# Performance work log

Measured on AMD Instinct MI355X. Metric: run time of the kernel, lower is better.

Reference implementation:

```python
import jax, jax.numpy as jnp
import numpy as np

HIDDEN = 1024
N_HEAD = 16
HEAD_DIM = HIDDEN // N_HEAD

def setup_inputs() -> dict:
    key = jax.random.key(0)
    ks = jax.random.split(key, 5)
    B, T = 2, 2048
    s_in = 1.0 / np.sqrt(HIDDEN)
    return {
        "x": jax.random.normal(ks[0], (B, T, HIDDEN), dtype=jnp.float32),
        "w_attn": jax.random.normal(ks[1], (HIDDEN, 3 * HIDDEN), dtype=jnp.float32) * s_in,
        "b_attn": jnp.zeros((3 * HIDDEN,), dtype=jnp.float32),
        "w_proj": jax.random.normal(ks[2], (HIDDEN, HIDDEN), dtype=jnp.float32) * s_in,
        "b_proj": jnp.zeros((HIDDEN,), dtype=jnp.float32),
    }

def reference(x, w_attn, b_attn, w_proj, b_proj):
    B, T, C = x.shape
    qkv = x @ w_attn + b_attn  # (B, T, 3C)
    q, k, v = jnp.split(qkv, 3, axis=-1)
    # (B, H, T, D)
    q = q.reshape(B, T, N_HEAD, HEAD_DIM).transpose(0, 2, 1, 3)
    k = k.reshape(B, T, N_HEAD, HEAD_DIM).transpose(0, 2, 1, 3)
    v = v.reshape(B, T, N_HEAD, HEAD_DIM).transpose(0, 2, 1, 3)
    scale = 1.0 / np.sqrt(HEAD_DIM).astype(np.float32)
    attn = jnp.einsum('bhqd,bhkd->bhqk', q, k) * scale
    causal = jnp.tril(jnp.ones((T, T), dtype=bool))
    attn = jnp.where(causal[None, None], attn, -jnp.inf)
    attn = jax.nn.softmax(attn, axis=-1)
    out = jnp.einsum('bhqk,bhkd->bhqd', attn, v)
    out = out.transpose(0, 2, 1, 3).reshape(B, T, C)
    return out @ w_proj + b_proj
```

## Files before the change

### kernel.cpp

```cpp
#include <hip/hip_runtime.h>
#include <stdint.h>

#define T_SEQ 2048
#define NB 2
#define NH 16
#define HD 64
#define HID 1024
#define MTOK (NB * T_SEQ)

typedef float f32x4 __attribute__((ext_vector_type(4)));
typedef float f32x16 __attribute__((ext_vector_type(16)));
typedef short bf16x8 __attribute__((ext_vector_type(8)));
typedef unsigned short u16;
typedef unsigned int u32;

#define QSCALE 0.1803368801f

__device__ __forceinline__ u16 f2bf(float f) {
  union { float f; uint32_t u; } v; v.f = f;
  return (u16)((v.u + 0x7fffu + ((v.u >> 16) & 1u)) >> 16);
}

__device__ __forceinline__ void gl_lds16(const void* g, void* l) {
  __builtin_amdgcn_global_load_lds(
      (const __attribute__((address_space(1))) unsigned int*)g,
      (__attribute__((address_space(3))) unsigned int*)l, 16, 0, 0);
}

__global__ __launch_bounds__(256)
void prep_k(const float* __restrict__ x, u16* __restrict__ xb,
            const float* __restrict__ wa, u16* __restrict__ waT,
            const float* __restrict__ wp, u16* __restrict__ wpT) {
  __shared__ float tile[32][33];
  const int bid = blockIdx.x, tid = threadIdx.x;
  if (bid < 1024) {
    int i = bid * 1024 + tid;
#pragma unroll
    for (int it = 0; it < 4; ++it, i += 256) {
      float4 f = ((const float4*)x)[i];
      ushort4 o;
      o.x = f2bf(f.x); o.y = f2bf(f.y); o.z = f2bf(f.z); o.w = f2bf(f.w);
      ((ushort4*)xb)[i] = o;
    }
    return;
  }
  const float* in;
  u16* out;
  int R, C, c0, r0;
  if (bid < 4096) {
    const int j = bid - 1024;
    in = wa; out = waT; R = HID; C = 3 * HID;
    c0 = (j % 96) * 32; r0 = (j / 96) * 32;
  } else {
    const int j = bid - 4096;
    in = wp; out = wpT; R = HID; C = HID;
    c0 = (j % 32) * 32; r0 = (j / 32) * 32;
  }
  const int tx = tid & 31, ty = tid >> 5;
#pragma unroll
  for (int i = 0; i < 32; i += 8)
    tile[ty + i][tx] = in[(size_t)(r0 + ty + i) * C + c0 + tx];
  __syncthreads();
#pragma unroll
  for (int i = 0; i < 32; i += 8)
    out[(size_t)(c0 + ty + i) * R + r0 + tx] = f2bf(tile[tx][ty + i]);
}

__global__ __launch_bounds__(512, 4)
void gemm_k(const u16* __restrict__ A, const u16* __restrict__ Bt,
            const float* __restrict__ bias,
            u16* __restrict__ q, u16* __restrict__ kk, u16* __restrict__ v) {
  __shared__ __align__(16) char lds[65536];
  const int tid = threadIdx.x, wid = tid >> 6, lane = tid & 63;
  const int bid = blockIdx.y * 24 + blockIdx.x;
  const int xcd = bid & 7, idx = bid >> 3;
  const int m0 = ((xcd >> 1) * 8 + idx / 12) * 128;
  const int n0 = ((xcd & 1) * 12 + idx % 12) * 128;
  const int wm = (wid >> 2) * 64, wn = (wid & 3) * 32;

  f32x4 acc[4][2];
  const f32x4 z = {0.f, 0.f, 0.f, 0.f};
#pragma unroll
  for (int mi = 0; mi < 4; ++mi)
#pragma unroll
    for (int ni = 0; ni < 2; ++ni) acc[mi][ni] = z;

  const int srow = tid >> 3;
  const int scsrc = ((((tid & 7) << 4) ^ ((srow & 7) << 4)) >> 1);
  const int rA = lane & 15;
  const int kg16 = (lane >> 4) << 4;

#define GSTAGE(tt_)                                                                     \
  do {                                                                                  \
    const int k0_ = (tt_) << 6;                                                         \
    char* base_ = lds + (((tt_) & 1) << 15);                                            \
    gl_lds16(A + (size_t)(m0 + srow) * HID + k0_ + scsrc, base_ + wid * 1024);          \
    gl_lds16(A + (size_t)(m0 + 64 + srow) * HID + k0_ + scsrc, base_ + 8192 + wid * 1024); \
    gl_lds16(Bt + (size_t)(n0 + srow) * HID + k0_ + scsrc, base_ + 16384 + wid * 1024); \
    gl_lds16(Bt + (size_t)(n0 + 64 + srow) * HID + k0_ + scsrc, base_ + 24576 + wid * 1024); \
  } while (0)

  GSTAGE(0);
  GSTAGE(1);

  for (int tt = 0; tt < 16; ++tt) {
    if (tt < 15) asm volatile("s_waitcnt vmcnt(4)" ::: "memory");
    else         asm volatile("s_waitcnt vmcnt(0)" ::: "memory");
    __builtin_amdgcn_s_barrier();
    __builtin_amdgcn_sched_barrier(0);

    const char* ab = lds + ((tt & 1) << 15);
    const char* bb = ab + 16384;
#pragma unroll
    for (int ks = 0; ks < 2; ++ks) {
      bf16x8 a[4], b[2];
#pragma unroll
      for (int mi = 0; mi < 4; ++mi) {
        const int row = wm + mi * 16 + rA;
        a[mi] = *(const bf16x8*)(ab + row * 128 + ((ks * 64 + kg16) ^ ((row & 7) << 4)));
      }
#pragma unroll
      for (int ni = 0; ni < 2; ++ni) {
        const int row = wn + ni * 16 + rA;
        b[ni] = *(const bf16x8*)(bb + row * 128 + ((ks * 64 + kg16) ^ ((row & 7) << 4)));
      }
#pragma unroll
      for (int mi = 0; mi < 4; ++mi)
#pragma unroll
        for (int ni = 0; ni < 2; ++ni)
          acc[mi][ni] = __builtin_amdgcn_mfma_f32_16x16x32_bf16(a[mi], b[ni], acc[mi][ni], 0, 0, 0);
    }

    __builtin_amdgcn_s_barrier();
    __builtin_amdgcn_sched_barrier(0);
    if (tt + 2 < 16) GSTAGE(tt + 2);
  }
#undef GSTAGE

  const int coll = lane & 15, rowl = (lane >> 4) << 2;
  const int reg = n0 >> 10;
  const int bb2 = m0 >> 11;
  const int tloc = (m0 & 2047) + wm;
  if (reg == 2) {
#pragma unroll
    for (int mi = 0; mi < 4; ++mi) {
#pragma unroll
      for (int ni = 0; ni < 2; ++ni) {
        const int n = n0 + wn + ni * 16 + coll;
        const float bv = bias[n];
        const int c = n & 1023, h = c >> 6, d = c & 63;
        ushort4 pk;
        pk.x = f2bf(acc[mi][ni][0] + bv);
        pk.y = f2bf(acc[mi][ni][1] + bv);
        pk.z = f2bf(acc[mi][ni][2] + bv);
        pk.w = f2bf(acc[mi][ni][3] + bv);
        const int t0 = tloc + mi * 16 + rowl;
        *(ushort4*)(v + ((size_t)(bb2 * NH + h) * HD + d) * T_SEQ + t0) = pk;
      }
    }
  } else {
    u16* dst = (reg == 0) ? q : kk;
    const float sc = (reg == 0) ? QSCALE : 1.0f;
#pragma unroll
    for (int mi = 0; mi < 4; ++mi) {
#pragma unroll
      for (int ni = 0; ni < 2; ++ni) {
        const int n = n0 + wn + ni * 16 + coll;
        const float bv = bias[n];
        const int c = n & 1023, h = c >> 6, d = c & 63;
#pragma unroll
        for (int r = 0; r < 4; ++r) {
          const int t = tloc + mi * 16 + rowl + r;
          dst[((size_t)(bb2 * NH + h) * T_SEQ + t) * HD + d] = f2bf((acc[mi][ni][r] + bv) * sc);
        }
      }
    }
  }
}

__global__ __launch_bounds__(512, 6)
void gemm2_k(const u16* __restrict__ A, const u16* __restrict__ Bt,
             const float* __restrict__ bias, float* __restrict__ outf) {
  __shared__ __align__(16) char lds[49152];
  const int tid = threadIdx.x, wid = tid >> 6, lane = tid & 63;
  const int m0 = blockIdx.y * 64, n0 = blockIdx.x * 128;
  const int wm = (wid >> 2) * 32, wn = (wid & 3) * 32;

  f32x4 acc[2][2];
  const f32x4 z = {0.f, 0.f, 0.f, 0.f};
#pragma unroll
  for (int mi = 0; mi < 2; ++mi)
#pragma unroll
    for (int ni = 0; ni < 2; ++ni) acc[mi][ni] = z;

  const int srow = tid >> 3;
  const int scsrc = ((((tid & 7) << 4) ^ ((srow & 7) << 4)) >> 1);
  const int rA = lane & 15;
  const int kg16 = (lane >> 4) << 4;

#define G2STAGE(tt_)                                                                    \
  do {                                                                                  \
    const int k0_ = (tt_) << 6;                                                         \
    char* base_ = lds + (((tt_) & 1) ? 24576 : 0);                                      \
    gl_lds16(A + (size_t)(m0 + srow) * HID + k0_ + scsrc, base_ + wid * 1024);          \
    gl_lds16(Bt + (size_t)(n0 + srow) * HID + k0_ + scsrc, base_ + 8192 + wid * 1024);  \
    gl_lds16(Bt + (size_t)(n0 + 64 + srow) * HID + k0_ + scsrc, base_ + 16384 + wid * 1024); \
  } while (0)

  G2STAGE(0);
  G2STAGE(1);

  for (int tt = 0; tt < 16; ++tt) {
    if (tt < 15) asm volatile("s_waitcnt vmcnt(3)" ::: "memory");
    else         asm volatile("s_waitcnt vmcnt(0)" ::: "memory");
    __builtin_amdgcn_s_barrier();
    __builtin_amdgcn_sched_barrier(0);

    const char* ab = lds + ((tt & 1) ? 24576 : 0);
    const char* bb = ab + 8192;
#pragma unroll
    for (int ks = 0; ks < 2; ++ks) {
      bf16x8 a[2], b[2];
#pragma unroll
      for (int mi = 0; mi < 2; ++mi) {
        const int row = wm + mi * 16 + rA;
        a[mi] = *(const bf16x8*)(ab + row * 128 + ((ks * 64 + kg16) ^ ((row & 7) << 4)));
      }
#pragma unroll
      for (int ni = 0; ni < 2; ++ni) {
        const int row = wn + ni * 16 + rA;
        b[ni] = *(const bf16x8*)(bb + row * 128 + ((ks * 64 + kg16) ^ ((row & 7) << 4)));
      }
#pragma unroll
      for (int mi = 0; mi < 2; ++mi)
#pragma unroll
        for (int ni = 0; ni < 2; ++ni)
          acc[mi][ni] = __builtin_amdgcn_mfma_f32_16x16x32_bf16(a[mi], b[ni], acc[mi][ni], 0, 0, 0);
    }

    __builtin_amdgcn_s_barrier();
    __builtin_amdgcn_sched_barrier(0);
    if (tt + 2 < 16) G2STAGE(tt + 2);
  }
#undef G2STAGE

  const int coll = lane & 15, rowl = (lane >> 4) << 2;
#pragma unroll
  for (int mi = 0; mi < 2; ++mi) {
#pragma unroll
    for (int ni = 0; ni < 2; ++ni) {
      const int n = n0 + wn + ni * 16 + coll;
      const float bv = bias[n];
#pragma unroll
      for (int r = 0; r < 4; ++r) {
        const int m = m0 + wm + mi * 16 + rowl + r;
        outf[(size_t)m * HID + n] = acc[mi][ni][r] + bv;
      }
    }
  }
}

__global__ __launch_bounds__(512, 4)
void attn_k(const u16* __restrict__ Q, const u16* __restrict__ K,
            const u16* __restrict__ Vt, u16* __restrict__ AO) {
  __shared__ __align__(16) char lds[65536];
  const int tid = threadIdx.x;
  const int lane = tid & 63;
  const int wid = tid >> 6;
  const int qsub = wid & 3, par = wid >> 2;
  const int bid = blockIdx.x;
  const int halfg = bid >> 8, r8 = bid & 255;
  const int bh = (r8 & 7) * 4 + ((r8 >> 3) & 3);
  const int lvl = r8 >> 5;
  const int qb = halfg ? lvl : (15 - lvl);
  const int q0 = qb * 128;
  const int ql = lane & 31, h = lane >> 5;
  const bool hi = (h != 0);

  const u16* Qg = Q + (size_t)bh * T_SEQ * HD;
  const u16* Kg = K + (size_t)bh * T_SEQ * HD;
  const u16* Vg = Vt + (size_t)bh * T_SEQ * HD;

  const int q0w = q0 + qsub * 32;
  const int dq = 2 * qb + (qsub >> 1);

  bf16x8 qf[4];
#pragma unroll
  for (int s = 0; s < 4; ++s)
    qf[s] = *(const bf16x8*)(Qg + (size_t)(q0w + ql) * HD + s * 16 + h * 8);

  f32x16 ot0, ot1;
#pragma unroll
  for (int i = 0; i < 16; ++i) { ot0[i] = 0.f; ot1[i] = 0.f; }
  float m = -3.0e38f, l = 0.f;

  const int srow = tid >> 3;
  const int scb = (tid & 7) << 4;
  const int sc0 = (scb ^ ((srow & 7) << 4)) >> 1;

  const int nsup = qb + 1;

#define STAGE(tt_)                                                            \
  do {                                                                        \
    const int kv0_ = (tt_) << 6;                                              \
    gl_lds16(Kg + (size_t)(kv0_ + srow) * HD + sc0,                           \
             lds + (((tt_) & 3) << 13) + wid * 1024);                         \
    gl_lds16(Vg + (size_t)srow * T_SEQ + kv0_ + sc0,                          \
             lds + 32768 + (((tt_) & 3) << 13) + wid * 1024);                 \
  } while (0)

  STAGE(0);
  STAGE(1);

  for (int ss = 0; ss < nsup; ++ss) {
    if (ss + 1 < nsup) {
      STAGE(2 * ss + 2);
      STAGE(2 * ss + 3);
      asm volatile("s_waitcnt vmcnt(4)" ::: "memory");
    } else {
      asm volatile("s_waitcnt vmcnt(0)" ::: "memory");
    }
    __builtin_amdgcn_s_barrier();
    __builtin_amdgcn_sched_barrier(0);

    const int tt = 2 * ss + par;
    if (tt <= dq) {
      const int kv0 = tt << 6;
      const char* kb = lds + ((tt & 3) << 13);
      const char* vb = lds + 32768 + ((tt & 3) << 13);
      f32x16 s0, s1;
#pragma unroll
      for (int i = 0; i < 16; ++i) { s0[i] = 0.f; s1[i] = 0.f; }
      __builtin_amdgcn_s_setprio(1);
#pragma unroll
      for (int s = 0; s < 4; ++s) {
        const int cb = 32 * s + 16 * h;
        const int r0 = ql, r1 = 32 + ql;
        bf16x8 kf0 = *(const bf16x8*)(kb + r0 * 128 + (cb ^ ((r0 & 7) << 4)));
        bf16x8 kf1 = *(const bf16x8*)(kb + r1 * 128 + (cb ^ ((r1 & 7) << 4)));
        s0 = __builtin_amdgcn_mfma_f32_32x32x16_bf16(kf0, qf[s], s0, 0, 0, 0);
        s1 = __builtin_amdgcn_mfma_f32_32x32x16_bf16(kf1, qf[s], s1, 0, 0, 0);
      }
      __builtin_amdgcn_s_setprio(0);
      if (tt == dq) {
        const int qg = q0w + ql;
#pragma unroll
        for (int r = 0; r < 16; ++r) {
          const int kvl = (r & 3) + 8 * (r >> 2) + 4 * h;
          if (kv0 + kvl > qg) s0[r] = -3.0e38f;
          if (kv0 + 32 + kvl > qg) s1[r] = -3.0e38f;
        }
      }
      float mx[16];
#pragma unroll
      for (int i = 0; i < 16; ++i) mx[i] = fmaxf(s0[i], s1[i]);
#pragma unroll
      for (int d = 8; d; d >>= 1)
#pragma unroll
        for (int i = 0; i < d; ++i) mx[i] = fmaxf(mx[i], mx[i + d]);
      const float tm = fmaxf(mx[0], __shfl_xor(mx[0], 32, 64));
      if (!__all(tm <= m + 4.0f)) {
        const float mnew = fmaxf(m, tm);
        const float fold = __builtin_amdgcn_exp2f(m - mnew);
        m = mnew;
        l *= fold;
#pragma unroll
        for (int i = 0; i < 16; ++i) { ot0[i] *= fold; ot1[i] *= fold; }
      }
#pragma unroll
      for (int i = 0; i < 16; ++i) {
        s0[i] = __builtin_amdgcn_exp2f(s0[i] - m);
        s1[i] = __builtin_amdgcn_exp2f(s1[i] - m);
      }
      float sm[16];
#pragma unroll
      for (int i = 0; i < 16; ++i) sm[i] = s0[i] + s1[i];
#pragma unroll
      for (int d = 8; d; d >>= 1)
#pragma unroll
        for (int i = 0; i < d; ++i) sm[i] += sm[i + d];
      l += sm[0] + __shfl_xor(sm[0], 32, 64);

      u32 w0[8], w1[8];
#pragma unroll
      for (int mm = 0; mm < 8; ++mm) {
        asm("v_cvt_pk_bf16_f32 %0, %1, %2" : "=v"(w0[mm]) : "v"(s0[2 * mm]), "v"(s0[2 * mm + 1]));
        asm("v_cvt_pk_bf16_f32 %0, %1, %2" : "=v"(w1[mm]) : "v"(s1[2 * mm]), "v"(s1[2 * mm + 1]));
      }
      __builtin_amdgcn_s_setprio(1);
#pragma unroll
      for (int sb = 0; sb < 2; ++sb) {
#pragma unroll
        for (int t = 0; t < 2; ++t) {
          u32 a0 = sb ? w1[4 * t]     : w0[4 * t];
          u32 a1 = sb ? w1[4 * t + 1] : w0[4 * t + 1];
          u32 a2 = sb ? w1[4 * t + 2] : w0[4 * t + 2];
          u32 a3 = sb ? w1[4 * t + 3] : w0[4 * t + 3];
          u32 snd0 = hi ? a0 : a2;
          u32 snd1 = hi ? a1 : a3;
          u32 own0 = hi ? a2 : a0;
          u32 own1 = hi ? a3 : a1;
          u32 p0 = __shfl_xor(snd0, 32, 64);
          u32 p1 = __shfl_xor(snd1, 32, 64);
          union { u32 u[4]; bf16x8 v; } fr;
          fr.u[0] = hi ? p0 : own0;
          fr.u[1] = hi ? p1 : own1;
          fr.u[2] = hi ? own0 : p0;
          fr.u[3] = hi ? own1 : p1;
          const int s = sb * 2 + t;
          const int cb = 32 * s + 16 * h;
          const int r0 = ql, r1 = 32 + ql;
          bf16x8 vf0 = *(const bf16x8*)(vb + r0 * 128 + (cb ^ ((r0 & 7) << 4)));
          bf16x8 vf1 = *(const bf16x8*)(vb + r1 * 128 + (cb ^ ((r1 & 7) << 4)));
          ot0 = __builtin_amdgcn_mfma_f32_32x32x16_bf16(vf0, fr.v, ot0, 0, 0, 0);
          ot1 = __builtin_amdgcn_mfma_f32_32x32x16_bf16(vf1, fr.v, ot1, 0, 0, 0);
        }
      }
      __builtin_amdgcn_s_setprio(0);
    }
    __builtin_amdgcn_s_barrier();
    __builtin_amdgcn_sched_barrier(0);
  }
#undef STAGE

  float* R = (float*)(lds + qsub * 8448);
  if (par == 1) {
#pragma unroll
    for (int r = 0; r < 16; ++r) {
      const int dl = (r & 3) + 8 * (r >> 2) + 4 * h;
      R[ql * 66 + dl] = ot0[r];
      R[ql * 66 + 32 + dl] = ot1[r];
    }
    if (!hi) { R[ql * 66 + 64] = m; R[ql * 66 + 65] = l; }
  }
  __builtin_amdgcn_s_barrier();
  if (par == 1) return;

  const float m2 = R[ql * 66 + 64];
  const float l2 = R[ql * 66 + 65];
  const float M = fmaxf(m, m2);
  const float c1 = __builtin_amdgcn_exp2f(m - M);
  const float c2 = __builtin_amdgcn_exp2f(m2 - M);
  const float L = c1 * l + c2 * l2;
  const float inv = 1.0f / L;
  float of0[16], of1[16];
#pragma unroll
  for (int r = 0; r < 16; ++r) {
    const int dl = (r & 3) + 8 * (r >> 2) + 4 * h;
    of0[r] = (c1 * ot0[r] + c2 * R[ql * 66 + dl]) * inv;
    of1[r] = (c1 * ot1[r] + c2 * R[ql * 66 + 32 + dl]) * inv;
  }
  asm volatile("s_waitcnt lgkmcnt(0)" ::: "memory");
  __builtin_amdgcn_sched_barrier(0);

  float* E = (float*)(lds + qsub * 8448);
#pragma unroll
  for (int r = 0; r < 16; ++r) {
    const int dl = (r & 3) + 8 * (r >> 2) + 4 * h;
    E[dl * 33 + ql] = of0[r];
    E[(dl + 32) * 33 + ql] = of1[r];
  }
  asm volatile("s_waitcnt lgkmcnt(0)" ::: "memory");
  __builtin_amdgcn_sched_barrier(0);
  const int bb = bh >> 4, hh = bh & 15;
  const int r2 = lane >> 3;
  const int c8 = (lane & 7) * 8;
#pragma unroll
  for (int g = 0; g < 4; ++g) {
    const int qrow = g * 8 + r2;
    union { u16 a[8]; bf16x8 v; } ov;
#pragma unroll
    for (int j = 0; j < 8; ++j) ov.a[j] = f2bf(E[(c8 + j) * 33 + qrow]);
    *(bf16x8*)(AO + (size_t)(bb * T_SEQ + q0 + qsub * 32 + qrow) * HID + hh * HD + c8) = ov.v;
  }
}

extern "C" void kernel_launch(void* const* d_in, const int* in_sizes, int n_in,
                              void* d_out, int out_size, void* d_ws, size_t ws_size,
                              hipStream_t stream) {
  const float* x      = (const float*)d_in[0];
  const float* w_attn = (const float*)d_in[1];
  const float* b_attn = (const float*)d_in[2];
  const float* w_proj = (const float*)d_in[3];
  const float* b_proj = (const float*)d_in[4];
  float* out = (float*)d_out;

  char* ws = (char*)d_ws;
  u16* xb   = (u16*)(ws);
  u16* wabT = (u16*)(ws + (size_t)(8  << 20));
  u16* wpbT = (u16*)(ws + (size_t)(14 << 20));
  u16* q    = (u16*)(ws + (size_t)(16 << 20));
  u16* k    = (u16*)(ws + (size_t)(24 << 20));
  u16* v    = (u16*)(ws + (size_t)(32 << 20));
  u16* ao   = (u16*)(ws + (size_t)(40 << 20));

  prep_k<<<dim3(5120), dim3(256), 0, stream>>>(x, xb, w_attn, wabT, w_proj, wpbT);
  gemm_k<<<dim3(24, 32), dim3(512), 0, stream>>>(xb, wabT, b_attn, q, k, v);
  attn_k<<<dim3(512), dim3(512), 0, stream>>>(q, k, v, ao);
  gemm2_k<<<dim3(8, 64), dim3(512), 0, stream>>>(ao, wpbT, b_proj, out);
}
```

Baseline: 89.00 us.

## Give each attention wave two query sub-tiles to reuse K/V fragments

The attention block drops from 8 waves to 4, and each wave now handles 64 query rows as two 32-row sets sharing the same K and V LDS fragments. K/V staging issues twice as many loads per thread to cover the tile, and the softmax/pack logic is factored into a helper run once per set. The intent is to halve LDS reads per MFMA and raise compute per wave. In exchange it doubles accumulator register pressure and cuts waves per block, which may lower occupancy and latency hiding.

```diff
diff --git a/kernel.cpp b/kernel.cpp
--- a/kernel.cpp
+++ b/kernel.cpp
@@ -260,14 +260,76 @@
   }
 }
 
-__global__ __launch_bounds__(512, 4)
+__device__ __forceinline__ void smxpack(f32x16& s0, f32x16& s1, float& m, float& l,
+                                        f32x16& ot0, f32x16& ot1, bf16x8* fr, bool hi) {
+  float mx[16];
+#pragma unroll
+  for (int i = 0; i < 16; ++i) mx[i] = fmaxf(s0[i], s1[i]);
+#pragma unroll
+  for (int d = 8; d; d >>= 1)
+#pragma unroll
+    for (int i = 0; i < d; ++i) mx[i] = fmaxf(mx[i], mx[i + d]);
+  const float tm = fmaxf(mx[0], __shfl_xor(mx[0], 32, 64));
+  if (!__all(tm <= m + 4.0f)) {
+    const float mnew = fmaxf(m, tm);
+    const float fold = __builtin_amdgcn_exp2f(m - mnew);
+    m = mnew;
+    l *= fold;
+#pragma unroll
+    for (int i = 0; i < 16; ++i) { ot0[i] *= fold; ot1[i] *= fold; }
+  }
+#pragma unroll
+  for (int i = 0; i < 16; ++i) {
+    s0[i] = __builtin_amdgcn_exp2f(s0[i] - m);
+    s1[i] = __builtin_amdgcn_exp2f(s1[i] - m);
+  }
+  float sm[16];
+#pragma unroll
+  for (int i = 0; i < 16; ++i) sm[i] = s0[i] + s1[i];
+#pragma unroll
+  for (int d = 8; d; d >>= 1)
+#pragma unroll
+    for (int i = 0; i < d; ++i) sm[i] += sm[i + d];
+  l += sm[0] + __shfl_xor(sm[0], 32, 64);
+
+  u32 w0[8], w1[8];
+#pragma unroll
+  for (int mm = 0; mm < 8; ++mm) {
+    asm("v_cvt_pk_bf16_f32 %0, %1, %2" : "=v"(w0[mm]) : "v"(s0[2 * mm]), "v"(s0[2 * mm + 1]));
+    asm("v_cvt_pk_bf16_f32 %0, %1, %2" : "=v"(w1[mm]) : "v"(s1[2 * mm]), "v"(s1[2 * mm + 1]));
+  }
+#pragma unroll
+  for (int sb = 0; sb < 2; ++sb) {
+#pragma unroll
+    for (int t = 0; t < 2; ++t) {
+      u32 a0 = sb ? w1[4 * t]     : w0[4 * t];
+      u32 a1 = sb ? w1[4 * t + 1] : w0[4 * t + 1];
+      u32 a2 = sb ? w1[4 * t + 2] : w0[4 * t + 2];
+      u32 a3 = sb ? w1[4 * t + 3] : w0[4 * t + 3];
+      u32 snd0 = hi ? a0 : a2;
+      u32 snd1 = hi ? a1 : a3;
+      u32 own0 = hi ? a2 : a0;
+      u32 own1 = hi ? a3 : a1;
+      u32 p0 = __shfl_xor(snd0, 32, 64);
+      u32 p1 = __shfl_xor(snd1, 32, 64);
+      union { u32 u[4]; bf16x8 v; } t2;
+      t2.u[0] = hi ? p0 : own0;
+      t2.u[1] = hi ? p1 : own1;
+      t2.u[2] = hi ? own0 : p0;
+      t2.u[3] = hi ? own1 : p1;
+      fr[sb * 2 + t] = t2.v;
+    }
+  }
+}
+
+__global__ __launch_bounds__(256, 2)
 void attn_k(const u16* __restrict__ Q, const u16* __restrict__ K,
             const u16* __restrict__ Vt, u16* __restrict__ AO) {
   __shared__ __align__(16) char lds[65536];
   const int tid = threadIdx.x;
   const int lane = tid & 63;
   const int wid = tid >> 6;
-  const int qsub = wid & 3, par = wid >> 2;
+  const int qsub = wid & 1, par = wid >> 1;
   const int bid = blockIdx.x;
   const int halfg = bid >> 8, r8 = bid & 255;
   const int bh = (r8 & 7) * 4 + ((r8 >> 3) & 3);
@@ -281,32 +343,35 @@
   const u16* Kg = K + (size_t)bh * T_SEQ * HD;
   const u16* Vg = Vt + (size_t)bh * T_SEQ * HD;
 
-  const int q0w = q0 + qsub * 32;
-  const int dq = 2 * qb + (qsub >> 1);
-
-  bf16x8 qf[4];
-#pragma unroll
-  for (int s = 0; s < 4; ++s)
-    qf[s] = *(const bf16x8*)(Qg + (size_t)(q0w + ql) * HD + s * 16 + h * 8);
-
-  f32x16 ot0, ot1;
-#pragma unroll
-  for (int i = 0; i < 16; ++i) { ot0[i] = 0.f; ot1[i] = 0.f; }
-  float m = -3.0e38f, l = 0.f;
+  const int q0w = q0 + qsub * 64;
+  const int dq = 2 * qb + qsub;
+
+  bf16x8 qfA[4], qfB[4];
+#pragma unroll
+  for (int s = 0; s < 4; ++s) {
+    qfA[s] = *(const bf16x8*)(Qg + (size_t)(q0w + ql) * HD + s * 16 + h * 8);
+    qfB[s] = *(const bf16x8*)(Qg + (size_t)(q0w + 32 + ql) * HD + s * 16 + h * 8);
+  }
+
+  f32x16 otA0, otA1, otB0, otB1;
+#pragma unroll
+  for (int i = 0; i < 16; ++i) { otA0[i] = 0.f; otA1[i] = 0.f; otB0[i] = 0.f; otB1[i] = 0.f; }
+  float mA = -3.0e38f, lA = 0.f, mB = -3.0e38f, lB = 0.f;
 
   const int srow = tid >> 3;
-  const int scb = (tid & 7) << 4;
-  const int sc0 = (scb ^ ((srow & 7) << 4)) >> 1;
+  const int sc0 = ((((tid & 7) << 4) ^ ((srow & 7) << 4)) >> 1);
 
   const int nsup = qb + 1;
 
 #define STAGE(tt_)                                                            \
   do {                                                                        \
     const int kv0_ = (tt_) << 6;                                              \
-    gl_lds16(Kg + (size_t)(kv0_ + srow) * HD + sc0,                           \
-             lds + (((tt_) & 3) << 13) + wid * 1024);                         \
-    gl_lds16(Vg + (size_t)srow * T_SEQ + kv0_ + sc0,                          \
-             lds + 32768 + (((tt_) & 3) << 13) + wid * 1024);                 \
+    char* kb_ = lds + (((tt_) & 3) << 13);                                    \
+    char* vb_ = lds + 32768 + (((tt_) & 3) << 13);                            \
+    gl_lds16(Kg + (size_t)(kv0_ + srow) * HD + sc0, kb_ + wid * 1024);        \
+    gl_lds16(Kg + (size_t)(kv0_ + 32 + srow) * HD + sc0, kb_ + 4096 + wid * 1024); \
+    gl_lds16(Vg + (size_t)srow * T_SEQ + kv0_ + sc0, vb_ + wid * 1024);       \
+    gl_lds16(Vg + (size_t)(32 + srow) * T_SEQ + kv0_ + sc0, vb_ + 4096 + wid * 1024); \
   } while (0)
 
   STAGE(0);
@@ -316,7 +381,7 @@
     if (ss + 1 < nsup) {
       STAGE(2 * ss + 2);
       STAGE(2 * ss + 3);
-      asm volatile("s_waitcnt vmcnt(4)" ::: "memory");
+      asm volatile("s_waitcnt vmcnt(8)" ::: "memory");
     } else {
       asm volatile("s_waitcnt vmcnt(0)" ::: "memory");
     }
@@ -328,93 +393,61 @@
       const int kv0 = tt << 6;
       const char* kb = lds + ((tt & 3) << 13);
       const char* vb = lds + 32768 + ((tt & 3) << 13);
-      f32x16 s0, s1;
-#pragma unroll
-      for (int i = 0; i < 16; ++i) { s0[i] = 0.f; s1[i] = 0.f; }
-      __builtin_amdgcn_s_setprio(1);
+      bf16x8 kf0[4], kf1[4];
 #pragma unroll
       for (int s = 0; s < 4; ++s) {
         const int cb = 32 * s + 16 * h;
         const int r0 = ql, r1 = 32 + ql;
-        bf16x8 kf0 = *(const bf16x8*)(kb + r0 * 128 + (cb ^ ((r0 & 7) << 4)));
-        bf16x8 kf1 = *(const bf16x8*)(kb + r1 * 128 + (cb ^ ((r1 & 7) << 4)));
-        s0 = __builtin_amdgcn_mfma_f32_32x32x16_bf16(kf0, qf[s], s0, 0, 0, 0);
-        s1 = __builtin_amdgcn_mfma_f32_32x32x16_bf16(kf1, qf[s], s1, 0, 0, 0);
+        kf0[s] = *(const bf16x8*)(kb + r0 * 128 + (cb ^ ((r0 & 7) << 4)));
+        kf1[s] = *(const bf16x8*)(kb + r1 * 128 + (cb ^ ((r1 & 7) << 4)));
+      }
+      f32x16 sA0, sA1, sB0, sB1;
+#pragma unroll
+      for (int i = 0; i < 16; ++i) { sA0[i] = 0.f; sA1[i] = 0.f; sB0[i] = 0.f; sB1[i] = 0.f; }
+      __builtin_amdgcn_s_setprio(1);
+#pragma unroll
+      for (int s = 0; s < 4; ++s) {
+        sA0 = __builtin_amdgcn_mfma_f32_32x32x16_bf16(kf0[s], qfA[s], sA0, 0, 0, 0);
+        sA1 = __builtin_amdgcn_mfma_f32_32x32x16_bf16(kf1[s], qfA[s], sA1, 0, 0, 0);
+      }
+#pragma unroll
+      for (int s = 0; s < 4; ++s) {
+        sB0 = __builtin_amdgcn_mfma_f32_32x32x16_bf16(kf0[s], qfB[s], sB0, 0, 0, 0);
+        sB1 = __builtin_amdgcn_mfma_f32_32x32x16_bf16(kf1[s], qfB[s], sB1, 0, 0, 0);
       }
       __builtin_amdgcn_s_setprio(0);
       if (tt == dq) {
-        const int qg = q0w + ql;
+        const int qgA = q0w + ql, qgB = q0w + 32 + ql;
 #pragma unroll
         for (int r = 0; r < 16; ++r) {
           const int kvl = (r & 3) + 8 * (r >> 2) + 4 * h;
-          if (kv0 + kvl > qg) s0[r] = -3.0e38f;
-          if (kv0 + 32 + kvl > qg) s1[r] = -3.0e38f;
+          if (kv0 + kvl > qgA) sA0[r] = -3.0e38f;
+          if (kv0 + 32 + kvl > qgA) sA1[r] = -3.0e38f;
+          if (kv0 + kvl > qgB) sB0[r] = -3.0e38f;
+          if (kv0 + 32 + kvl > qgB) sB1[r] = -3.0e38f;
         }
       }
-      float mx[16];
-#pragma unroll
-      for (int i = 0; i < 16; ++i) mx[i] = fmaxf(s0[i], s1[i]);
-#pragma unroll
-      for (int d = 8; d; d >>= 1)
-#pragma unroll
-        for (int i = 0; i < d; ++i) mx[i] = fmaxf(mx[i], mx[i + d]);
-      const float tm = fmaxf(mx[0], __shfl_xor(mx[0], 32, 64));
-      if (!__all(tm <= m + 4.0f)) {
-        const float mnew = fmaxf(m, tm);
-        const float fold = __builtin_amdgcn_exp2f(m - mnew);
-        m = mnew;
-        l *= fold;
-#pragma unroll
-        for (int i = 0; i < 16; ++i) { ot0[i] *= fold; ot1[i] *= fold; }
-      }
-#pragma unroll
-      for (int i = 0; i < 16; ++i) {
-        s0[i] = __builtin_amdgcn_exp2f(s0[i] - m);
-        s1[i] = __builtin_amdgcn_exp2f(s1[i] - m);
-      }
-      float sm[16];
-#pragma unroll
-      for (int i = 0; i < 16; ++i) sm[i] = s0[i] + s1[i];
-#pragma unroll
-      for (int d = 8; d; d >>= 1)
-#pragma unroll
-        for (int i = 0; i < d; ++i) sm[i] += sm[i + d];
-      l += sm[0] + __shfl_xor(sm[0], 32, 64);
-
-      u32 w0[8], w1[8];
-#pragma unroll
-      for (int mm = 0; mm < 8; ++mm) {
-        asm("v_cvt_pk_bf16_f32 %0, %1, %2" : "=v"(w0[mm]) : "v"(s0[2 * mm]), "v"(s0[2 * mm + 1]));
-        asm("v_cvt_pk_bf16_f32 %0, %1, %2" : "=v"(w1[mm]) : "v"(s1[2 * mm]), "v"(s1[2 * mm + 1]));
+      bf16x8 frA[4], frB[4];
+      smxpack(sA0, sA1, mA, lA, otA0, otA1, frA, hi);
+      smxpack(sB0, sB1, mB, lB, otB0, otB1, frB, hi);
+      bf16x8 vf0[4], vf1[4];
+#pragma unroll
+      for (int s = 0; s < 4; ++s) {
+        const int cb = 32 * s + 16 * h;
+        const int r0 = ql, r1 = 32 + ql;
+        vf0[s] = *(const bf16x8*)(vb + r0 * 128 + (cb ^ ((r0 & 7) << 4)));
+        vf1[s] = *(const bf16x8*)(vb + r1 * 128 + (cb ^ ((r1 & 7) << 4)));
       }
       __builtin_amdgcn_s_setprio(1);
 #pragma unroll
-      for (int sb = 0; sb < 2; ++sb) {
-#pragma unroll
-        for (int t = 0; t < 2; ++t) {
-          u32 a0 = sb ? w1[4 * t]     : w0[4 * t];
-          u32 a1 = sb ? w1[4 * t + 1] : w0[4 * t + 1];
-          u32 a2 = sb ? w1[4 * t + 2] : w0[4 * t + 2];
-          u32 a3 = sb ? w1[4 * t + 3] : w0[4 * t + 3];
-          u32 snd0 = hi ? a0 : a2;
-          u32 snd1 = hi ? a1 : a3;
-          u32 own0 = hi ? a2 : a0;
-          u32 own1 = hi ? a3 : a1;
-          u32 p0 = __shfl_xor(snd0, 32, 64);
-          u32 p1 = __shfl_xor(snd1, 32, 64);
-          union { u32 u[4]; bf16x8 v; } fr;
-          fr.u[0] = hi ? p0 : own0;
-          fr.u[1] = hi ? p1 : own1;
-          fr.u[2] = hi ? own0 : p0;
-          fr.u[3] = hi ? own1 : p1;
-          const int s = sb * 2 + t;
-          const int cb = 32 * s + 16 * h;
-          const int r0 = ql, r1 = 32 + ql;
-          bf16x8 vf0 = *(const bf16x8*)(vb + r0 * 128 + (cb ^ ((r0 & 7) << 4)));
-          bf16x8 vf1 = *(const bf16x8*)(vb + r1 * 128 + (cb ^ ((r1 & 7) << 4)));
-          ot0 = __builtin_amdgcn_mfma_f32_32x32x16_bf16(vf0, fr.v, ot0, 0, 0, 0);
-          ot1 = __builtin_amdgcn_mfma_f32_32x32x16_bf16(vf1, fr.v, ot1, 0, 0, 0);
-        }
+      for (int s = 0; s < 4; ++s) {
+        otA0 = __builtin_amdgcn_mfma_f32_32x32x16_bf16(vf0[s], frA[s], otA0, 0, 0, 0);
+        otA1 = __builtin_amdgcn_mfma_f32_32x32x16_bf16(vf1[s], frA[s], otA1, 0, 0, 0);
+      }
+#pragma unroll
+      for (int s = 0; s < 4; ++s) {
+        otB0 = __builtin_amdgcn_mfma_f32_32x32x16_bf16(vf0[s], frB[s], otB0, 0, 0, 0);
+        otB1 = __builtin_amdgcn_mfma_f32_32x32x16_bf16(vf1[s], frB[s], otB1, 0, 0, 0);
       }
       __builtin_amdgcn_s_setprio(0);
     }
@@ -423,56 +456,66 @@
   }
 #undef STAGE
 
-  float* R = (float*)(lds + qsub * 8448);
   if (par == 1) {
 #pragma unroll
-    for (int r = 0; r < 16; ++r) {
-      const int dl = (r & 3) + 8 * (r >> 2) + 4 * h;
-      R[ql * 66 + dl] = ot0[r];
-      R[ql * 66 + 32 + dl] = ot1[r];
-    }
-    if (!hi) { R[ql * 66 + 64] = m; R[ql * 66 + 65] = l; }
+    for (int set = 0; set < 2; ++set) {
+      float* R = (float*)(lds + (qsub * 2 + set) * 8448);
+      const f32x16& o0 = set ? otB0 : otA0;
+      const f32x16& o1 = set ? otB1 : otA1;
+#pragma unroll
+      for (int r = 0; r < 16; ++r) {
+        const int dl = (r & 3) + 8 * (r >> 2) + 4 * h;
+        R[ql * 66 + dl] = o0[r];
+        R[ql * 66 + 32 + dl] = o1[r];
+      }
+      if (!hi) { R[ql * 66 + 64] = set ? mB : mA; R[ql * 66 + 65] = set ? lB : lA; }
+    }
   }
   __builtin_amdgcn_s_barrier();
   if (par == 1) return;
 
-  const float m2 = R[ql * 66 + 64];
-  const float l2 = R[ql * 66 + 65];
-  const float M = fmaxf(m, m2);
-  const float c1 = __builtin_amdgcn_exp2f(m - M);
-  const float c2 = __builtin_amdgcn_exp2f(m2 - M);
-  const float L = c1 * l + c2 * l2;
-  const float inv = 1.0f / L;
-  float of0[16], of1[16];
-#pragma unroll
-  for (int r = 0; r < 16; ++r) {
-    const int dl = (r & 3) + 8 * (r >> 2) + 4 * h;
-    of0[r] = (c1 * ot0[r] + c2 * R[ql * 66 + dl]) * inv;
-    of1[r] = (c1 * ot1[r] + c2 * R[ql * 66 + 32 + dl]) * inv;
-  }
-  asm volatile("s_waitcnt lgkmcnt(0)" ::: "memory");
-  __builtin_amdgcn_sched_barrier(0);
-
-  float* E = (float*)(lds + qsub * 8448);
-#pragma unroll
-  for (int r = 0; r < 16; ++r) {
-    const int dl = (r & 3) + 8 * (r >> 2) + 4 * h;
-    E[dl * 33 + ql] = of0[r];
-    E[(dl + 32) * 33 + ql] = of1[r];
-  }
-  asm volatile("s_waitcnt lgkmcnt(0)" ::: "memory");
-  __builtin_amdgcn_sched_barrier(0);
   const int bb = bh >> 4, hh = bh & 15;
   const int r2 = lane >> 3;
   const int c8 = (lane & 7) * 8;
-#pragma unroll
-  for (int g = 0; g < 4; ++g) {
-    const int qrow = g * 8 + r2;
-    union { u16 a[8]; bf16x8 v; } ov;
-#pragma unroll
-    for (int j = 0; j < 8; ++j) ov.a[j] = f2bf(E[(c8 + j) * 33 + qrow]);
-    *(bf16x8*)(AO + (size_t)(bb * T_SEQ + q0 + qsub * 32 + qrow) * HID + hh * HD + c8) = ov.v;
-  }
+
+  auto finish = [&](int set, float m_, float l_, const f32x16& o0, const f32x16& o1) {
+    float* R = (float*)(lds + (qsub * 2 + set) * 8448);
+    const float m2 = R[ql * 66 + 64];
+    const float l2 = R[ql * 66 + 65];
+    const float M = fmaxf(m_, m2);
+    const float c1 = __builtin_amdgcn_exp2f(m_ - M);
+    const float c2 = __builtin_amdgcn_exp2f(m2 - M);
+    const float L = c1 * l_ + c2 * l2;
+    const float inv = 1.0f / L;
+    float of0[16], of1[16];
+#pragma unroll
+    for (int r = 0; r < 16; ++r) {
+      const int dl = (r & 3) + 8 * (r >> 2) + 4 * h;
+      of0[r] = (c1 * o0[r] + c2 * R[ql * 66 + dl]) * inv;
+      of1[r] = (c1 * o1[r] + c2 * R[ql * 66 + 32 + dl]) * inv;
+    }
+    asm volatile("s_waitcnt lgkmcnt(0)" ::: "memory");
+    __builtin_amdgcn_sched_barrier(0);
+    float* E = R;
+#pragma unroll
+    for (int r = 0; r < 16; ++r) {
+      const int dl = (r & 3) + 8 * (r >> 2) + 4 * h;
+      E[dl * 33 + ql] = of0[r];
+      E[(dl + 32) * 33 + ql] = of1[r];
+    }
+    asm volatile("s_waitcnt lgkmcnt(0)" ::: "memory");
+    __builtin_amdgcn_sched_barrier(0);
+#pragma unroll
+    for (int g = 0; g < 4; ++g) {
+      const int qrow = g * 8 + r2;
+      union { u16 a[8]; bf16x8 v; } ov;
+#pragma unroll
+      for (int j = 0; j < 8; ++j) ov.a[j] = f2bf(E[(c8 + j) * 33 + qrow]);
+      *(bf16x8*)(AO + (size_t)(bb * T_SEQ + q0 + qsub * 64 + set * 32 + qrow) * HID + hh * HD + c8) = ov.v;
+    }
+  };
+  finish(0, mA, lA, otA0, otA1);
+  finish(1, mB, lB, otB0, otB1);
 }
 
 extern "C" void kernel_launch(void* const* d_in, const int* in_sizes, int n_in,
@@ -496,6 +539,6 @@
 
   prep_k<<<dim3(5120), dim3(256), 0, stream>>>(x, xb, w_attn, wabT, w_proj, wpbT);
   gemm_k<<<dim3(24, 32), dim3(512), 0, stream>>>(xb, wabT, b_attn, q, k, v);
-  attn_k<<<dim3(512), dim3(512), 0, stream>>>(q, k, v, ao);
+  attn_k<<<dim3(512), dim3(256), 0, stream>>>(q, k, v, ao);
   gemm2_k<<<dim3(8, 64), dim3(512), 0, stream>>>(ao, wpbT, b_proj, out);
 }
```

Result: slower. 94.20 us (+5.8%).
